# Kernel tuning notes

Measured on AMD Instinct MI355X. Metric: run time of the kernel, lower is better.

Reference implementation:

```python
import jax, jax.numpy as jnp
import numpy as np

EPS = 1e-08


def _stats(x):
    # x: [B, L, C] -> stats: [B, 6*C]
    B, L, C = x.shape
    mean = jnp.mean(x, axis=1)                                   # [B, C]
    std = jnp.std(x, axis=1, ddof=1) + EPS                       # torch.std is unbiased
    skew = jnp.mean((x - mean[:, None, :]) ** 3, axis=1) / std ** 3
    diff_std = jnp.std(x[:, 1:, :] - x[:, :-1, :], axis=1, ddof=1)
    recent_start = max(1, L - L // 4)
    recent = x[:, recent_start:, :]
    recent_mean = jnp.mean(recent, axis=1)
    recent_std = jnp.std(recent, axis=1, ddof=1) + EPS
    return jnp.concatenate([mean, std, skew, diff_std, recent_mean, recent_std], axis=-1)


def setup_inputs() -> dict:
    key = jax.random.key(0)
    ks = jax.random.split(key, 7)
    B, L, C = 64, 4096, 128
    nf = 6 * C
    x = jax.random.normal(ks[0], (B, L, C), dtype=jnp.float32)
    # Linear weights stored as [in, out] for x @ W + b
    W1 = jax.random.normal(ks[1], (nf, 128), dtype=jnp.float32) * (1.0 / np.sqrt(nf))
    b1 = jnp.zeros((128,), dtype=jnp.float32)
    W2 = jax.random.normal(ks[2], (128, 32), dtype=jnp.float32) * (1.0 / np.sqrt(128))
    b2 = jnp.zeros((32,), dtype=jnp.float32)
    W3 = jax.random.normal(ks[3], (32, C), dtype=jnp.float32) * (1.0 / np.sqrt(32))
    b3 = jnp.zeros((C,), dtype=jnp.float32)
    return {"x": x, "W1": W1, "b1": b1, "W2": W2, "b2": b2, "W3": W3, "b3": b3}


def reference(x, W1, b1, W2, b2, W3, b3):
    stats = _stats(x)                                            # [B, 6C]
    h = jax.nn.gelu(stats @ W1 + b1, approximate=False)          # dropout is identity at eval
    h = jax.nn.gelu(h @ W2 + b2, approximate=False)
    alpha = jax.nn.sigmoid(h @ W3 + b3)                          # [B, C]
    return alpha
```

## Files before the change

kernel.cpp:

```cpp
#include <hip/hip_runtime.h>
#include <math.h>

#define BATCH 64
#define LSEQ 4096
#define CH 128
#define NCHUNK 32
#define CHROWS (LSEQ / NCHUNK)
#define TROWS (CHROWS / 8)
#define NRECENT 1024

__global__ __launch_bounds__(256) void k_stats_partial(
    const float* __restrict__ x, float* __restrict__ ws) {
  const int tid = threadIdx.x;
  const int c4 = tid & 31;
  const int ty = tid >> 5;
  const int chk = blockIdx.x;
  const int b = blockIdx.y;
  const int ts = chk * CHROWS + ty * TROWS;

  const float4* px =
      reinterpret_cast<const float4*>(x + ((size_t)b * LSEQ + ts) * CH) + c4;
  const int rowstep = CH / 4;

  float sx[4] = {0, 0, 0, 0}, sx2[4] = {0, 0, 0, 0}, sx3[4] = {0, 0, 0, 0};
  float sd2[4] = {0, 0, 0, 0};
  float pv[4], first[4], sd[4];

  float4 v0 = px[0];
  pv[0] = first[0] = v0.x;
  pv[1] = first[1] = v0.y;
  pv[2] = first[2] = v0.z;
  pv[3] = first[3] = v0.w;
#pragma unroll
  for (int k = 0; k < 4; k++) {
    float f = pv[k], ff = f * f;
    sx[k] += f; sx2[k] += ff; sx3[k] = fmaf(ff, f, sx3[k]);
  }
#pragma unroll 5
  for (int i = 1; i < TROWS; i++) {
    float4 u = px[i * rowstep];
    float cur[4] = {u.x, u.y, u.z, u.w};
#pragma unroll
    for (int k = 0; k < 4; k++) {
      float f = cur[k], ff = f * f;
      sx[k] += f; sx2[k] += ff; sx3[k] = fmaf(ff, f, sx3[k]);
      float d = f - pv[k];
      sd2[k] = fmaf(d, d, sd2[k]);
      pv[k] = f;
    }
  }
  if (ts + TROWS < LSEQ) {
    float4 u = px[TROWS * rowstep];
    float cur[4] = {u.x, u.y, u.z, u.w};
#pragma unroll
    for (int k = 0; k < 4; k++) {
      float d = cur[k] - pv[k];
      sd2[k] = fmaf(d, d, sd2[k]);
      sd[k] = cur[k] - first[k];
    }
  } else {
#pragma unroll
    for (int k = 0; k < 4; k++) sd[k] = pv[k] - first[k];
  }

  float vals[20];
#pragma unroll
  for (int k = 0; k < 4; k++) {
    vals[0 + k] = sx[k];
    vals[4 + k] = sx2[k];
    vals[8 + k] = sx3[k];
    vals[12 + k] = sd[k];
    vals[16 + k] = sd2[k];
  }
#pragma unroll
  for (int j = 0; j < 20; j++) vals[j] += __shfl_xor(vals[j], 32);

  __shared__ float4 red[5][4][32];
  const int w = tid >> 6;
  const int lane = tid & 63;
  if (lane < 32) {
#pragma unroll
    for (int s = 0; s < 5; s++)
      red[s][w][c4] = make_float4(vals[s * 4 + 0], vals[s * 4 + 1],
                                  vals[s * 4 + 2], vals[s * 4 + 3]);
  }
  __syncthreads();
  if (tid < 160) {
    const int s = tid >> 5, c = tid & 31;
    float4 r = red[s][0][c];
    float4 r1 = red[s][1][c], r2 = red[s][2][c], r3 = red[s][3][c];
    r.x += r1.x + r2.x + r3.x;
    r.y += r1.y + r2.y + r3.y;
    r.z += r1.z + r2.z + r3.z;
    r.w += r1.w + r2.w + r3.w;
    float* wsb = ws + ((size_t)(b * NCHUNK + chk) * 5 + s) * CH;
    reinterpret_cast<float4*>(wsb)[c] = r;
  }
}

__global__ __launch_bounds__(1024) void k_stats_mlp(
    const float* __restrict__ ws,
    const float* __restrict__ W1, const float* __restrict__ b1,
    const float* __restrict__ W2, const float* __restrict__ b2,
    const float* __restrict__ W3, const float* __restrict__ b3,
    float* __restrict__ out) {
  const int b = blockIdx.x;
  const int tid = threadIdx.x;
  const int f = tid & 127;
  const int g = tid >> 7;

  __shared__ float part[5][8][CH];
  __shared__ float stats[6 * CH];
  __shared__ float h1p[8][128];
  __shared__ float h1[128];
  __shared__ float h2p[32][32];
  __shared__ float h2[32];
  __shared__ float l3p[8][128];

  {
    float t0 = 0, t1 = 0, t2 = 0, t3 = 0, t4 = 0;
#pragma unroll
    for (int chk = g * 4; chk < g * 4 + 4; chk++) {
      const float* p = ws + ((size_t)(b * NCHUNK + chk) * 5) * CH + f;
      t0 += p[0 * CH];
      t1 += p[1 * CH];
      t2 += p[2 * CH];
      t3 += p[3 * CH];
      t4 += p[4 * CH];
    }
    part[0][g][f] = t0;
    part[1][g][f] = t1;
    part[2][g][f] = t2;
    part[3][g][f] = t3;
    part[4][g][f] = t4;
  }
  __syncthreads();

  if (tid < CH) {
    float t0 = 0, t1 = 0, t2 = 0, t3 = 0, t4 = 0, t5 = 0, t6 = 0;
#pragma unroll
    for (int k = 0; k < 8; k++) {
      float a0 = part[0][k][tid], a1 = part[1][k][tid];
      t0 += a0; t1 += a1;
      t2 += part[2][k][tid];
      t3 += part[3][k][tid];
      t4 += part[4][k][tid];
      if (k >= 6) { t5 += a0; t6 += a1; }
    }

    const float Lf = (float)LSEQ;
    float mean = t0 / Lf;
    float var = fmaxf(t1 - Lf * mean * mean, 0.f) / (Lf - 1.f);
    float stdE = sqrtf(var) + 1e-8f;
    float m3 = t2 / Lf - 3.f * mean * (t1 / Lf) + 2.f * mean * mean * mean;
    float skew = m3 / (stdE * stdE * stdE);
    const float nd = (float)(LSEQ - 1);
    float dmean = t3 / nd;
    float dvar = fmaxf(t4 - nd * dmean * dmean, 0.f) / (nd - 1.f);
    float dstd = sqrtf(dvar);
    const float nr = (float)NRECENT;
    float rmean = t5 / nr;
    float rvar = fmaxf(t6 - nr * rmean * rmean, 0.f) / (nr - 1.f);
    float rstd = sqrtf(rvar) + 1e-8f;

    stats[0 * CH + tid] = mean;
    stats[1 * CH + tid] = stdE;
    stats[2 * CH + tid] = skew;
    stats[3 * CH + tid] = dstd;
    stats[4 * CH + tid] = rmean;
    stats[5 * CH + tid] = rstd;
  }
  __syncthreads();

  {
    const int k0 = 96 * g;
    float a0 = 0, a1 = 0, a2 = 0, a3 = 0;
#pragma unroll 6
    for (int k = 0; k < 96; k += 4) {
      a0 = fmaf(stats[k0 + k + 0], W1[(size_t)(k0 + k + 0) * 128 + f], a0);
      a1 = fmaf(stats[k0 + k + 1], W1[(size_t)(k0 + k + 1) * 128 + f], a1);
      a2 = fmaf(stats[k0 + k + 2], W1[(size_t)(k0 + k + 2) * 128 + f], a2);
      a3 = fmaf(stats[k0 + k + 3], W1[(size_t)(k0 + k + 3) * 128 + f], a3);
    }
    h1p[g][f] = (a0 + a1) + (a2 + a3);
  }
  __syncthreads();
  if (tid < CH) {
    float a = b1[tid];
#pragma unroll
    for (int k = 0; k < 8; k++) a += h1p[k][tid];
    h1[tid] = 0.5f * a * (1.f + erff(a * 0.70710678118654752f));
  }
  __syncthreads();

  {
    const int f2 = tid & 31, p2 = tid >> 5;
    float a0 = 0, a1 = 0;
#pragma unroll
    for (int k = 4 * p2; k < 4 * p2 + 4; k += 2) {
      a0 = fmaf(h1[k], W2[k * 32 + f2], a0);
      a1 = fmaf(h1[k + 1], W2[(k + 1) * 32 + f2], a1);
    }
    h2p[p2][f2] = a0 + a1;
  }
  __syncthreads();
  if (tid < 32) {
    float a = b2[tid];
#pragma unroll
    for (int p2 = 0; p2 < 32; p2++) a += h2p[p2][tid];
    h2[tid] = 0.5f * a * (1.f + erff(a * 0.70710678118654752f));
  }
  __syncthreads();

  {
    float a0 = 0, a1 = 0;
#pragma unroll
    for (int j = 4 * g; j < 4 * g + 4; j += 2) {
      a0 = fmaf(h2[j], W3[j * 128 + f], a0);
      a1 = fmaf(h2[j + 1], W3[(j + 1) * 128 + f], a1);
    }
    l3p[g][f] = a0 + a1;
  }
  __syncthreads();
  if (tid < CH) {
    float a = b3[tid];
#pragma unroll
    for (int k = 0; k < 8; k++) a += l3p[k][tid];
    out[(size_t)b * CH + tid] = 1.f / (1.f + expf(-a));
  }
}

extern "C" void kernel_launch(void* const* d_in, const int* in_sizes, int n_in,
                              void* d_out, int out_size, void* d_ws,
                              size_t ws_size, hipStream_t stream) {
  const float* x = (const float*)d_in[0];
  const float* W1 = (const float*)d_in[1];
  const float* b1 = (const float*)d_in[2];
  const float* W2 = (const float*)d_in[3];
  const float* b2 = (const float*)d_in[4];
  const float* W3 = (const float*)d_in[5];
  const float* b3 = (const float*)d_in[6];
  float* out = (float*)d_out;
  float* ws = (float*)d_ws;

  dim3 g1(NCHUNK, BATCH);
  k_stats_partial<<<g1, 256, 0, stream>>>(x, ws);
  k_stats_mlp<<<BATCH, 1024, 0, stream>>>(ws, W1, b1, W2, b2, W3, b3, out);
}
```

Measured before the change: 36.39 us.

## Fuse stats reduction and MLP into one kernel per batch

Merges the chunked partial-statistics kernel and the MLP kernel into one kernel with one 1024-thread block per batch row. Each block streams the whole sequence for its batch and reduces in shared memory, which removes the workspace round trip and the second launch. The cost is that the grid shrinks to 64 blocks, so most compute units sit idle during the memory-bound streaming phase.

```diff
diff --git a/kernel.cpp b/kernel.cpp
--- a/kernel.cpp
+++ b/kernel.cpp
@@ -4,149 +4,118 @@
 #define BATCH 64
 #define LSEQ 4096
 #define CH 128
-#define NCHUNK 32
-#define CHROWS (LSEQ / NCHUNK)
-#define TROWS (CHROWS / 8)
+#define NTG 32
+#define GROWS (LSEQ / NTG)
 #define NRECENT 1024
 
-__global__ __launch_bounds__(256) void k_stats_partial(
-    const float* __restrict__ x, float* __restrict__ ws) {
-  const int tid = threadIdx.x;
-  const int c4 = tid & 31;
-  const int ty = tid >> 5;
-  const int chk = blockIdx.x;
-  const int b = blockIdx.y;
-  const int ts = chk * CHROWS + ty * TROWS;
-
-  const float4* px =
-      reinterpret_cast<const float4*>(x + ((size_t)b * LSEQ + ts) * CH) + c4;
-  const int rowstep = CH / 4;
-
-  float sx[4] = {0, 0, 0, 0}, sx2[4] = {0, 0, 0, 0}, sx3[4] = {0, 0, 0, 0};
-  float sd2[4] = {0, 0, 0, 0};
-  float pv[4], first[4], sd[4];
-
-  float4 v0 = px[0];
-  pv[0] = first[0] = v0.x;
-  pv[1] = first[1] = v0.y;
-  pv[2] = first[2] = v0.z;
-  pv[3] = first[3] = v0.w;
-#pragma unroll
-  for (int k = 0; k < 4; k++) {
-    float f = pv[k], ff = f * f;
-    sx[k] += f; sx2[k] += ff; sx3[k] = fmaf(ff, f, sx3[k]);
-  }
-#pragma unroll 5
-  for (int i = 1; i < TROWS; i++) {
-    float4 u = px[i * rowstep];
-    float cur[4] = {u.x, u.y, u.z, u.w};
-#pragma unroll
-    for (int k = 0; k < 4; k++) {
-      float f = cur[k], ff = f * f;
-      sx[k] += f; sx2[k] += ff; sx3[k] = fmaf(ff, f, sx3[k]);
-      float d = f - pv[k];
-      sd2[k] = fmaf(d, d, sd2[k]);
-      pv[k] = f;
-    }
-  }
-  if (ts + TROWS < LSEQ) {
-    float4 u = px[TROWS * rowstep];
-    float cur[4] = {u.x, u.y, u.z, u.w};
-#pragma unroll
-    for (int k = 0; k < 4; k++) {
-      float d = cur[k] - pv[k];
-      sd2[k] = fmaf(d, d, sd2[k]);
-      sd[k] = cur[k] - first[k];
-    }
-  } else {
-#pragma unroll
-    for (int k = 0; k < 4; k++) sd[k] = pv[k] - first[k];
-  }
-
-  float vals[20];
-#pragma unroll
-  for (int k = 0; k < 4; k++) {
-    vals[0 + k] = sx[k];
-    vals[4 + k] = sx2[k];
-    vals[8 + k] = sx3[k];
-    vals[12 + k] = sd[k];
-    vals[16 + k] = sd2[k];
-  }
-#pragma unroll
-  for (int j = 0; j < 20; j++) vals[j] += __shfl_xor(vals[j], 32);
-
-  __shared__ float4 red[5][4][32];
-  const int w = tid >> 6;
-  const int lane = tid & 63;
-  if (lane < 32) {
-#pragma unroll
-    for (int s = 0; s < 5; s++)
-      red[s][w][c4] = make_float4(vals[s * 4 + 0], vals[s * 4 + 1],
-                                  vals[s * 4 + 2], vals[s * 4 + 3]);
-  }
-  __syncthreads();
-  if (tid < 160) {
-    const int s = tid >> 5, c = tid & 31;
-    float4 r = red[s][0][c];
-    float4 r1 = red[s][1][c], r2 = red[s][2][c], r3 = red[s][3][c];
-    r.x += r1.x + r2.x + r3.x;
-    r.y += r1.y + r2.y + r3.y;
-    r.z += r1.z + r2.z + r3.z;
-    r.w += r1.w + r2.w + r3.w;
-    float* wsb = ws + ((size_t)(b * NCHUNK + chk) * 5 + s) * CH;
-    reinterpret_cast<float4*>(wsb)[c] = r;
-  }
-}
-
-__global__ __launch_bounds__(1024) void k_stats_mlp(
-    const float* __restrict__ ws,
+__global__ __launch_bounds__(1024) void k_all(
+    const float* __restrict__ x,
     const float* __restrict__ W1, const float* __restrict__ b1,
     const float* __restrict__ W2, const float* __restrict__ b2,
     const float* __restrict__ W3, const float* __restrict__ b3,
     float* __restrict__ out) {
+  const int tid = threadIdx.x;
+  const int c4 = tid & 31;
+  const int tg = tid >> 5;
   const int b = blockIdx.x;
-  const int tid = threadIdx.x;
-  const int f = tid & 127;
-  const int g = tid >> 7;
-
-  __shared__ float part[5][8][CH];
+  const int ts = tg * GROWS;
+
+  __shared__ float red[5][16][CH];
+  __shared__ float fold[5][CH];
+  __shared__ float rfold[2][CH];
   __shared__ float stats[6 * CH];
-  __shared__ float h1p[8][128];
-  __shared__ float h1[128];
+  __shared__ float h1p[8][CH];
+  __shared__ float h1[CH];
   __shared__ float h2p[32][32];
   __shared__ float h2[32];
-  __shared__ float l3p[8][128];
-
-  {
-    float t0 = 0, t1 = 0, t2 = 0, t3 = 0, t4 = 0;
-#pragma unroll
-    for (int chk = g * 4; chk < g * 4 + 4; chk++) {
-      const float* p = ws + ((size_t)(b * NCHUNK + chk) * 5) * CH + f;
-      t0 += p[0 * CH];
-      t1 += p[1 * CH];
-      t2 += p[2 * CH];
-      t3 += p[3 * CH];
-      t4 += p[4 * CH];
-    }
-    part[0][g][f] = t0;
-    part[1][g][f] = t1;
-    part[2][g][f] = t2;
-    part[3][g][f] = t3;
-    part[4][g][f] = t4;
+  __shared__ float l3p[8][CH];
+
+  {
+    const float4* px =
+        reinterpret_cast<const float4*>(x + ((size_t)b * LSEQ + ts) * CH) + c4;
+    const int rowstep = CH / 4;
+
+    float sx[4] = {0, 0, 0, 0}, sx2[4] = {0, 0, 0, 0}, sx3[4] = {0, 0, 0, 0};
+    float sd2[4] = {0, 0, 0, 0};
+    float pv[4], first[4], sd[4];
+
+    float4 v0 = px[0];
+    pv[0] = first[0] = v0.x;
+    pv[1] = first[1] = v0.y;
+    pv[2] = first[2] = v0.z;
+    pv[3] = first[3] = v0.w;
+#pragma unroll
+    for (int k = 0; k < 4; k++) {
+      float f = pv[k], ff = f * f;
+      sx[k] += f; sx2[k] += ff; sx3[k] = fmaf(ff, f, sx3[k]);
+    }
+#pragma unroll 8
+    for (int i = 1; i < GROWS; i++) {
+      float4 u = px[i * rowstep];
+      float cur[4] = {u.x, u.y, u.z, u.w};
+#pragma unroll
+      for (int k = 0; k < 4; k++) {
+        float f = cur[k], ff = f * f;
+        sx[k] += f; sx2[k] += ff; sx3[k] = fmaf(ff, f, sx3[k]);
+        float d = f - pv[k];
+        sd2[k] = fmaf(d, d, sd2[k]);
+        pv[k] = f;
+      }
+    }
+    if (tg < NTG - 1) {
+      float4 u = px[GROWS * rowstep];
+      float cur[4] = {u.x, u.y, u.z, u.w};
+#pragma unroll
+      for (int k = 0; k < 4; k++) {
+        float d = cur[k] - pv[k];
+        sd2[k] = fmaf(d, d, sd2[k]);
+        sd[k] = cur[k] - first[k];
+      }
+    } else {
+#pragma unroll
+      for (int k = 0; k < 4; k++) sd[k] = pv[k] - first[k];
+    }
+
+    float vals[20];
+#pragma unroll
+    for (int k = 0; k < 4; k++) {
+      vals[0 + k] = sx[k];
+      vals[4 + k] = sx2[k];
+      vals[8 + k] = sx3[k];
+      vals[12 + k] = sd[k];
+      vals[16 + k] = sd2[k];
+    }
+#pragma unroll
+    for (int j = 0; j < 20; j++) vals[j] += __shfl_xor(vals[j], 32);
+
+    const int w = tid >> 6;
+    if ((tid & 63) < 32) {
+#pragma unroll
+      for (int s = 0; s < 5; s++)
+        reinterpret_cast<float4*>(red[s][w])[c4] =
+            make_float4(vals[s * 4 + 0], vals[s * 4 + 1],
+                        vals[s * 4 + 2], vals[s * 4 + 3]);
+    }
+  }
+  __syncthreads();
+
+  if (tid < 640) {
+    const int s = tid >> 7, c = tid & 127;
+    float t = 0;
+#pragma unroll
+    for (int w = 0; w < 16; w++) t += red[s][w][c];
+    fold[s][c] = t;
+    if (s < 2) {
+      float r = red[s][12][c] + red[s][13][c] + red[s][14][c] + red[s][15][c];
+      rfold[s][c] = r;
+    }
   }
   __syncthreads();
 
   if (tid < CH) {
-    float t0 = 0, t1 = 0, t2 = 0, t3 = 0, t4 = 0, t5 = 0, t6 = 0;
-#pragma unroll
-    for (int k = 0; k < 8; k++) {
-      float a0 = part[0][k][tid], a1 = part[1][k][tid];
-      t0 += a0; t1 += a1;
-      t2 += part[2][k][tid];
-      t3 += part[3][k][tid];
-      t4 += part[4][k][tid];
-      if (k >= 6) { t5 += a0; t6 += a1; }
-    }
+    float t0 = fold[0][tid], t1 = fold[1][tid], t2 = fold[2][tid];
+    float t3 = fold[3][tid], t4 = fold[4][tid];
+    float t5 = rfold[0][tid], t6 = rfold[1][tid];
 
     const float Lf = (float)LSEQ;
     float mean = t0 / Lf;
@@ -172,6 +141,9 @@
   }
   __syncthreads();
 
+  const int f = tid & 127;
+  const int g = tid >> 7;
+
   {
     const int k0 = 96 * g;
     float a0 = 0, a1 = 0, a2 = 0, a3 = 0;
@@ -241,9 +213,6 @@
   const float* W3 = (const float*)d_in[5];
   const float* b3 = (const float*)d_in[6];
   float* out = (float*)d_out;
-  float* ws = (float*)d_ws;
-
-  dim3 g1(NCHUNK, BATCH);
-  k_stats_partial<<<g1, 256, 0, stream>>>(x, ws);
-  k_stats_mlp<<<BATCH, 1024, 0, stream>>>(ws, W1, b1, W2, b2, W3, b3, out);
+
+  k_all<<<BATCH, 1024, 0, stream>>>(x, W1, b1, W2, b2, W3, b3, out);
 }
```

After: 39.92 us. +9.7%, slower.
